# Performance work log

Measured on AMD Instinct MI355X. Metric: run time of the kernel, lower is better.

## Reference

```python
import jax, jax.numpy as jnp
import numpy as np

N_NODES = 10000
N_EDGES = 160000
N_GRAPHS = 20
IN_F, HID, OUT_F, HEADS = 50, 256, 121, 4
NEG_SLOPE = 0.2
GN_EPS = 1e-5
SM_EPS = 1e-16


def _with_self_loops(edge_index, n):
    loop = jnp.arange(n, dtype=edge_index.dtype)
    src = jnp.concatenate([edge_index[0], loop])
    dst = jnp.concatenate([edge_index[1], loop])
    return src, dst


def gat_conv(x, W, att_src, att_dst, bias, src, dst, heads, out_c):
    # PyG GATConv: linear -> per-node attention halves -> edge leaky_relu
    # -> softmax over incoming edges of each dst -> weighted scatter-sum.
    n = x.shape[0]
    h = (x @ W).reshape(n, heads, out_c)                # [N,H,C]
    a_s = (h * att_src).sum(-1)                          # [N,H]
    a_d = (h * att_dst).sum(-1)                          # [N,H]
    e = a_s[src] + a_d[dst]                              # [E,H]
    e = jnp.where(e > 0, e, NEG_SLOPE * e)
    e_max = jax.ops.segment_max(e, dst, num_segments=n)  # self-loops cover all dst
    ex = jnp.exp(e - e_max[dst])
    den = jax.ops.segment_sum(ex, dst, num_segments=n)
    alpha = ex / (den[dst] + SM_EPS)                     # [E,H]
    out = jax.ops.segment_sum(h[src] * alpha[..., None], dst, num_segments=n)
    return out.reshape(n, heads * out_c) + bias


def graph_norm(x, batch, weight, bias, mean_scale, n_graphs):
    cnt = jax.ops.segment_sum(jnp.ones((x.shape[0],), x.dtype), batch,
                              num_segments=n_graphs)[:, None]    # [G,1]
    mean = jax.ops.segment_sum(x, batch, num_segments=n_graphs) / cnt
    ctr = x - mean[batch] * mean_scale
    var = jax.ops.segment_sum(ctr * ctr, batch, num_segments=n_graphs) / cnt
    inv = jax.lax.rsqrt(var + GN_EPS)
    return weight * ctr * inv[batch] + bias


def setup_inputs() -> dict:
    key = jax.random.key(0)
    ks = jax.random.split(key, 24)
    d = {}
    d['x'] = jax.random.normal(ks[0], (N_NODES, IN_F), jnp.float32)
    d['edge_index'] = jax.random.randint(ks[1], (2, N_EDGES), 0, N_NODES, jnp.int64 if jax.config.jax_enable_x64 else jnp.int32)
    d['batch'] = jnp.sort(jax.random.randint(ks[2], (N_NODES,), 0, N_GRAPHS))
    def glorot(k, shape):
        fan = shape[0] + shape[-1]
        return jax.random.normal(k, shape, jnp.float32) * np.sqrt(2.0 / fan)
    dims = [(IN_F, HEADS, HID), (HEADS * HID, HEADS, HID), (HEADS * HID, HEADS, HID), (HEADS * HID, 1, OUT_F)]
    i = 3
    for li, (fin, h, c) in enumerate(dims, 1):
        d[f'W{li}'] = glorot(ks[i], (fin, h * c)); i += 1
        d[f'as{li}'] = glorot(ks[i], (h, c)); i += 1
        d[f'ad{li}'] = glorot(ks[i], (h, c)); i += 1
        d[f'b{li}'] = jnp.zeros((h * c,), jnp.float32)
    for li in (1, 2, 3):
        w = HEADS * HID
        d[f'gw{li}'] = jnp.ones((w,), jnp.float32)
        d[f'gb{li}'] = jnp.zeros((w,), jnp.float32)
        d[f'ga{li}'] = jnp.ones((w,), jnp.float32)
    return d


def reference(x, edge_index, batch,
              W1, as1, ad1, b1, W2, as2, ad2, b2, W3, as3, ad3, b3, W4, as4, ad4, b4,
              gw1, gb1, ga1, gw2, gb2, ga2, gw3, gb3, ga3):
    src, dst = _with_self_loops(edge_index, N_NODES)
    h = gat_conv(x, W1, as1, ad1, b1, src, dst, HEADS, HID)
    h = jax.nn.elu(graph_norm(h, batch, gw1, gb1, ga1, N_GRAPHS))
    h = gat_conv(h, W2, as2, ad2, b2, src, dst, HEADS, HID)
    h = jax.nn.elu(graph_norm(h, batch, gw2, gb2, ga2, N_GRAPHS))
    h = gat_conv(h, W3, as3, ad3, b3, src, dst, HEADS, HID)
    h = jax.nn.elu(graph_norm(h, batch, gw3, gb3, ga3, N_GRAPHS))
    return gat_conv(h, W4, as4, ad4, b4, src, dst, 1, OUT_F)
```

## Files before the change

### kernel.cpp

```cpp
#include <hip/hip_runtime.h>
#include <math.h>

#define NN 10000
#define NE 160000
#define E2 (NE + NN)
#define NG 20
#define MPAD 10240
#define NSPLIT 8

typedef __attribute__((ext_vector_type(8))) short short8;
typedef __attribute__((ext_vector_type(4))) float f32x4;

__device__ inline unsigned short f2bf(float f){
  unsigned u = __float_as_uint(f);
  unsigned r = u + 0x7FFFu + ((u >> 16) & 1u);
  return (unsigned short)(r >> 16);
}
__device__ inline float bf2f(unsigned short h){ return __uint_as_float(((unsigned)h) << 16); }

__device__ inline void gload_lds16(const void* g, void* l){
  __builtin_amdgcn_global_load_lds((const __attribute__((address_space(1))) void*)g,
                                   (__attribute__((address_space(3))) void*)l, 16, 0, 0);
}

__global__ void k_gptr(const int* __restrict__ batch, int* __restrict__ gptr){
  int g = threadIdx.x;
  if (g > NG) return;
  int lo = 0, hi = NN;
  while (lo < hi){ int mid = (lo+hi)>>1; if (batch[mid] < g) lo = mid+1; else hi = mid; }
  gptr[g] = lo;
}

__global__ void k_count(const int* __restrict__ ei, int* __restrict__ cnt){
  int e = blockIdx.x*256 + threadIdx.x;
  if (e >= E2) return;
  int d = (e < NE) ? ei[NE + e] : (e - NE);
  atomicAdd(&cnt[d], 1);
}

__global__ void k_scan(const int* __restrict__ cnt, int* __restrict__ ptr){
  __shared__ int tpre[256];
  __shared__ int tsum[256];
  int tid = threadIdx.x;
  const int per = (NN + 255)/256;
  int base = tid*per;
  int s = 0;
  for (int i=0;i<per;i++){ int idx=base+i; if (idx<NN) s += cnt[idx]; }
  tsum[tid] = s;
  __syncthreads();
  if (tid == 0){
    int run = 0;
    for (int i=0;i<256;i++){ tpre[i]=run; run += tsum[i]; }
    ptr[NN] = run;
  }
  __syncthreads();
  int run = tpre[tid];
  for (int i=0;i<per;i++){ int idx=base+i; if (idx<NN){ ptr[idx]=run; run += cnt[idx]; } }
}

__global__ void k_copy(const int* __restrict__ src, int* __restrict__ dst){
  int i = blockIdx.x*256 + threadIdx.x;
  if (i < NN) dst[i] = src[i];
}

__global__ void k_scatter(const int* __restrict__ ei, int* __restrict__ fill, int* __restrict__ csrc){
  int e = blockIdx.x*256 + threadIdx.x;
  if (e >= E2) return;
  int s, d;
  if (e < NE){ s = ei[e]; d = ei[NE + e]; } else { s = d = e - NE; }
  int pos = atomicAdd(&fill[d], 1);
  csrc[pos] = s;
}

__global__ void k_xconv(const float* __restrict__ x, unsigned short* __restrict__ xbf){
  int i = blockIdx.x*256 + threadIdx.x;
  if (i >= MPAD*64) return;
  int r = i >> 6, c = i & 63;
  float v = (r < NN && c < 50) ? x[r*50 + c] : 0.f;
  xbf[i] = f2bf(v);
}

#define WT0 0
#define WT1 65536
#define WT2 1114112
#define WT3 2162688
#define WTT 2293760
__global__ void k_wconvall(const float* __restrict__ W0, const float* __restrict__ W1,
                           const float* __restrict__ W2, const float* __restrict__ W3,
                           unsigned short* __restrict__ wt){
  int i = blockIdx.x*256 + threadIdx.x;
  if (i >= WTT) return;
  const float* W; int K, N, Kpad, off;
  if (i < WT1){ W=W0; K=50; N=1024; Kpad=64; off=WT0; }
  else if (i < WT2){ W=W1; K=1024; N=1024; Kpad=1024; off=WT1; }
  else if (i < WT3){ W=W2; K=1024; N=1024; Kpad=1024; off=WT2; }
  else { W=W3; K=1024; N=121; Kpad=1024; off=WT3; }
  int j = i - off;
  int nn = j / Kpad, kk = j - nn*Kpad;
  float v = (nn < N && kk < K) ? W[(size_t)kk*N + nn] : 0.f;
  wt[i] = f2bf(v);
}

template<int TBN>
__global__ __launch_bounds__(512, 2) void k_gemm256(
    const unsigned short* __restrict__ A,
    const unsigned short* __restrict__ Bt,
    unsigned short* __restrict__ Cbf,
    int M, int K, int FS, int ncb)
{
  constexpr int MFR = 8;
  constexpr int NFR = TBN/64;
  constexpr int ABYTES = 256*64;
  constexpr int BBYTES = TBN*64;
  constexpr int AINST = 2;
  constexpr int BINST = TBN/128;
  constexpr int LPS = AINST + BINST;
  __shared__ unsigned short sA[3*256*32];
  __shared__ unsigned short sB[3*TBN*32];
  const int tid = threadIdx.x;
  const int wave = tid >> 6;
  const int lane = tid & 63;
  const int nwg = gridDim.x;
  const int q = nwg >> 3, rmod = nwg & 7;
  const int xcd = blockIdx.x & 7, idx = blockIdx.x >> 3;
  const int wg = (xcd < rmod) ? (xcd*(q+1) + idx) : (rmod*(q+1) + (xcd - rmod)*q + idx);
  const int rowt = wg / ncb;
  const int colt = wg - rowt*ncb;
  const int row0 = rowt * 256;
  const int col0 = colt * TBN;
  const int wr = (wave >> 2) * 128;
  const int wc = (wave & 3) * (TBN/4);
  f32x4 acc[MFR][NFR];
  #pragma unroll
  for (int i=0;i<MFR;i++)
    #pragma unroll
    for (int j=0;j<NFR;j++){ acc[i][j][0]=0.f; acc[i][j][1]=0.f; acc[i][j][2]=0.f; acc[i][j][3]=0.f; }

  const unsigned short* aP[AINST];
  int aL[AINST];
  #pragma unroll
  for (int i=0;i<AINST;i++){
    int s = (wave*AINST + i)*64 + lane;
    int row = s >> 2, chn = (s & 3) ^ ((row >> 1) & 3);
    aP[i] = A + (size_t)(row0 + row)*K + chn*8;
    aL[i] = (wave*AINST + i)*1024;
  }
  const unsigned short* bP[BINST];
  int bL[BINST];
  #pragma unroll
  for (int i=0;i<BINST;i++){
    int s = (wave*BINST + i)*64 + lane;
    int row = s >> 2, chn = (s & 3) ^ ((row >> 1) & 3);
    bP[i] = Bt + (size_t)(col0 + row)*K + chn*8;
    bL[i] = (wave*BINST + i)*1024;
  }
  char* ldsA = (char*)sA;
  char* ldsB = (char*)sB;

  auto STAGE = [&](int k0, int buf){
    #pragma unroll
    for (int i=0;i<AINST;i++) gload_lds16(aP[i] + k0, ldsA + buf*ABYTES + aL[i]);
    #pragma unroll
    for (int i=0;i<BINST;i++) gload_lds16(bP[i] + k0, ldsB + buf*BBYTES + bL[i]);
  };

  const int NT = K >> 5;
  const int kch = lane >> 4;
  const int rlo = lane & 15;

  STAGE(0, 0);
  STAGE(32, 1);

  int cur = 0;
  for (int t = 0; t < NT; ++t){
    asm volatile("s_waitcnt lgkmcnt(0)" ::: "memory");
    if (t+1 < NT){
      if constexpr (LPS==4) asm volatile("s_waitcnt vmcnt(4)" ::: "memory");
      else                  asm volatile("s_waitcnt vmcnt(3)" ::: "memory");
    } else {
      asm volatile("s_waitcnt vmcnt(0)" ::: "memory");
    }
    __builtin_amdgcn_sched_barrier(0);
    __builtin_amdgcn_s_barrier();
    __builtin_amdgcn_sched_barrier(0);
    const unsigned short* bA = sA + cur*(256*32);
    const unsigned short* bB = sB + cur*(TBN*32);
    short8 af[MFR], bfr[NFR];
    #pragma unroll
    for (int m=0;m<MFR;m++){
      int r = wr + m*16 + rlo;
      af[m] = *(const short8*)(bA + r*32 + ((kch ^ ((r>>1)&3))<<3));
    }
    #pragma unroll
    for (int n=0;n<NFR;n++){
      int r = wc + n*16 + rlo;
      bfr[n] = *(const short8*)(bB + r*32 + ((kch ^ ((r>>1)&3))<<3));
    }
    if (t+2 < NT){
      int nb = cur + 2; if (nb >= 3) nb -= 3;
      STAGE((t+2) << 5, nb);
    }
    __builtin_amdgcn_s_setprio(1);
    #pragma unroll
    for (int m=0;m<MFR;m++)
      #pragma unroll
      for (int n=0;n<NFR;n++)
        acc[m][n] = __builtin_amdgcn_mfma_f32_16x16x32_bf16(af[m], bfr[n], acc[m][n], 0, 0, 0);
    __builtin_amdgcn_s_setprio(0);
    cur += 1; if (cur == 3) cur = 0;
  }
  const int cr = (lane >> 4) * 4;
  const int cc = lane & 15;
  #pragma unroll
  for (int m=0;m<MFR;m++){
    #pragma unroll
    for (int n=0;n<NFR;n++){
      int col = col0 + wc + n*16 + cc;
      #pragma unroll
      for (int r=0;r<4;r++){
        int row = row0 + wr + m*16 + cr + r;
        if (row < M) Cbf[(size_t)row*FS + col] = f2bf(acc[m][n][r]);
      }
    }
  }
}

__global__ __launch_bounds__(256) void k_attprepw(
    const unsigned short* __restrict__ h,
    const float* __restrict__ atts, const float* __restrict__ attd,
    float* __restrict__ a_s, float* __restrict__ a_d)
{
  const int wid = threadIdx.x >> 6, lane = threadIdx.x & 63;
  const int node = blockIdx.x*4 + wid;
  const unsigned short* hp = h + (size_t)node*1024 + lane*16;
  short8 v0 = *(const short8*)hp;
  short8 v1 = *(const short8*)(hp+8);
  const float* sp = atts + lane*16;
  const float* dp = attd + lane*16;
  float ss = 0.f, sd = 0.f;
  #pragma unroll
  for (int j=0;j<8;j++){ float f = bf2f((unsigned short)v0[j]); ss += f*sp[j];   sd += f*dp[j]; }
  #pragma unroll
  for (int j=0;j<8;j++){ float f = bf2f((unsigned short)v1[j]); ss += f*sp[8+j]; sd += f*dp[8+j]; }
  #pragma unroll
  for (int o=8;o;o>>=1){ ss += __shfl_xor(ss,o); sd += __shfl_xor(sd,o); }
  if ((lane & 15) == 0){
    int hh = lane >> 4;
    a_s[node*4 + hh] = ss;
    a_d[node*4 + hh] = sd;
  }
}

__global__ __launch_bounds__(256) void k_attprep4(
    const unsigned short* __restrict__ h,
    const float* __restrict__ atts, const float* __restrict__ attd,
    float* __restrict__ a_s, float* __restrict__ a_d)
{
  const int wid = threadIdx.x >> 6, lane = threadIdx.x & 63;
  const int node = blockIdx.x*4 + wid;
  const unsigned short* hp = h + (size_t)node*128;
  float ss = 0.f, sd = 0.f;
  {
    float f = bf2f(hp[lane]);
    if (lane < 121){ ss += f*atts[lane]; sd += f*attd[lane]; }
  }
  int c2 = lane + 64;
  if (c2 < 121){
    float f = bf2f(hp[c2]);
    ss += f*atts[c2]; sd += f*attd[c2];
  }
  #pragma unroll
  for (int o=32;o;o>>=1){ ss += __shfl_xor(ss,o); sd += __shfl_xor(sd,o); }
  if (lane == 0){ a_s[node] = ss; a_d[node] = sd; }
}

__global__ __launch_bounds__(256) void k_gatherw(
    const unsigned short* __restrict__ h,
    const float* __restrict__ a_s, const float* __restrict__ a_d,
    const int* __restrict__ ptr, const int* __restrict__ csrc,
    const float* __restrict__ bias, float* __restrict__ out)
{
  __shared__ float sal[4][64*4];
  __shared__ int ssn[4][64];
  const int wid = threadIdx.x >> 6, lane = threadIdx.x & 63;
  const int node = blockIdx.x*4 + wid;
  const int hh = lane >> 4;
  const int beg = ptr[node], deg = ptr[node+1] - beg;
  f32x4 ad4 = *(const f32x4*)(a_d + node*4);
  float acc[16], acc2[16];
  #pragma unroll
  for (int j=0;j<16;j++){ acc[j]=0.f; acc2[j]=0.f; }
  f32x4 denp = {0.f,0.f,0.f,0.f};
  const unsigned short* hb = h + lane*16;

  for (int c0 = 0; c0 < deg; c0 += 64){
    int n = min(64, deg - c0);
    if (lane < n){
      int s = csrc[beg + c0 + lane];
      f32x4 as4 = *(const f32x4*)(a_s + s*4);
      f32x4 e4;
      #pragma unroll
      for (int k2=0;k2<4;k2++){
        float ev = as4[k2] + ad4[k2];
        ev = ev > 0.f ? ev : 0.2f*ev;
        float x = __expf(ev);
        e4[k2] = x;
        denp[k2] += x;
      }
      *(f32x4*)&sal[wid][lane*4] = e4;
      ssn[wid][lane] = s;
    }
    int e = 0;
    for (; e + 1 < n; e += 2){
      int sA_ = ssn[wid][e], sB_ = ssn[wid][e+1];
      float aA = sal[wid][e*4 + hh], aB = sal[wid][(e+1)*4 + hh];
      const unsigned short* pA = hb + (size_t)sA_*1024;
      const unsigned short* pB = hb + (size_t)sB_*1024;
      short8 uA0 = *(const short8*)pA, uA1 = *(const short8*)(pA+8);
      short8 uB0 = *(const short8*)pB, uB1 = *(const short8*)(pB+8);
      #pragma unroll
      for (int j=0;j<8;j++){ acc[j]   += bf2f((unsigned short)uA0[j])*aA;
                             acc[8+j] += bf2f((unsigned short)uA1[j])*aA; }
      #pragma unroll
      for (int j=0;j<8;j++){ acc2[j]   += bf2f((unsigned short)uB0[j])*aB;
                             acc2[8+j] += bf2f((unsigned short)uB1[j])*aB; }
    }
    if (e < n){
      int sA_ = ssn[wid][e];
      float aA = sal[wid][e*4 + hh];
      const unsigned short* pA = hb + (size_t)sA_*1024;
      short8 uA0 = *(const short8*)pA, uA1 = *(const short8*)(pA+8);
      #pragma unroll
      for (int j=0;j<8;j++){ acc[j]   += bf2f((unsigned short)uA0[j])*aA;
                             acc[8+j] += bf2f((unsigned short)uA1[j])*aA; }
    }
  }
  #pragma unroll
  for (int o=32;o;o>>=1){
    #pragma unroll
    for (int k2=0;k2<4;k2++) denp[k2] += __shfl_xor(denp[k2], o);
  }
  float inv = 1.f / (denp[hh] + 1e-16f);
  float* op = out + (size_t)node*1024 + lane*16;
  const float* bp = bias + lane*16;
  #pragma unroll
  for (int j=0;j<16;j++) op[j] = (acc[j]+acc2[j])*inv + bp[j];
}

__global__ __launch_bounds__(256) void k_gatherw1(
    const unsigned short* __restrict__ h,
    const float* __restrict__ a_s, const float* __restrict__ a_d,
    const int* __restrict__ ptr, const int* __restrict__ csrc,
    const float* __restrict__ bias, float* __restrict__ out)
{
  __shared__ float sal[4][64];
  __shared__ int ssn[4][64];
  const int wid = threadIdx.x >> 6, lane = threadIdx.x & 63;
  const int node = blockIdx.x*4 + wid;
  const int beg = ptr[node], deg = ptr[node+1] - beg;
  float ad = a_d[node];
  float den = 0.f;
  float acc[2] = {0.f,0.f}, acc2[2] = {0.f,0.f};
  const int c0i = lane*2;
  const unsigned short* hb = h + c0i;

  for (int b0 = 0; b0 < deg; b0 += 64){
    int n = min(64, deg - b0);
    if (lane < n){
      int s = csrc[beg + b0 + lane];
      float ev = a_s[s] + ad;
      ev = ev > 0.f ? ev : 0.2f*ev;
      float x = __expf(ev);
      sal[wid][lane] = x;
      ssn[wid][lane] = s;
      den += x;
    }
    int e = 0;
    for (; e + 1 < n; e += 2){
      int sA_ = ssn[wid][e], sB_ = ssn[wid][e+1];
      float aA = sal[wid][e], aB = sal[wid][e+1];
      const unsigned short* pA = hb + (size_t)sA_*128;
      const unsigned short* pB = hb + (size_t)sB_*128;
      acc[0]  += bf2f(pA[0])*aA; acc[1]  += bf2f(pA[1])*aA;
      acc2[0] += bf2f(pB[0])*aB; acc2[1] += bf2f(pB[1])*aB;
    }
    if (e < n){
      int sA_ = ssn[wid][e];
      float aA = sal[wid][e];
      const unsigned short* pA = hb + (size_t)sA_*128;
      acc[0] += bf2f(pA[0])*aA; acc[1] += bf2f(pA[1])*aA;
    }
  }
  #pragma unroll
  for (int o=32;o;o>>=1) den += __shfl_xor(den, o);
  float inv = 1.f / (den + 1e-16f);
  if (c0i < 121)   out[(size_t)node*121 + c0i]   = (acc[0]+acc2[0])*inv + bias[c0i];
  if (c0i+1 < 121) out[(size_t)node*121 + c0i+1] = (acc[1]+acc2[1])*inv + bias[c0i+1];
}

__global__ void k_gnstats(const float* __restrict__ x, const int* __restrict__ gptr,
                          float* __restrict__ psum, float* __restrict__ psq){
  int g = blockIdx.x, cc = blockIdx.y, sp = blockIdx.z;
  int c = cc*256 + threadIdx.x;
  int beg = gptr[g], end = gptr[g+1];
  int n = end - beg;
  int per = (n + NSPLIT - 1) / NSPLIT;
  int nb = beg + sp*per, ne = min(end, nb + per);
  float s = 0.f, qv = 0.f;
  for (int i = nb; i < ne; i++){ float v = x[(size_t)i*1024 + c]; s += v; qv += v*v; }
  int idx = (sp*NG + g)*1024 + c;
  psum[idx] = s; psq[idx] = qv;
}

__global__ void k_coef(const float* __restrict__ psum, const float* __restrict__ psq,
                       const int* __restrict__ gptr,
                       const float* __restrict__ w, const float* __restrict__ b, const float* __restrict__ ms,
                       float* __restrict__ cA, float* __restrict__ cB){
  int i = blockIdx.x*256 + threadIdx.x;
  if (i >= NG*1024) return;
  int g = i >> 10, c = i & 1023;
  float cntf = (float)(gptr[g+1] - gptr[g]);
  float sm = 0.f, sq = 0.f;
  #pragma unroll
  for (int sp=0; sp<NSPLIT; sp++){
    sm += psum[(sp*NG + g)*1024 + c];
    sq += psq[(sp*NG + g)*1024 + c];
  }
  float m = sm / cntf;
  float s = ms[c];
  float ex2 = sq / cntf;
  float var = ex2 - 2.f*s*m*m + s*s*m*m;
  float inv = rsqrtf(var + 1e-5f);
  float wa = w[c]*inv;
  cA[i] = wa;
  cB[i] = b[c] - wa*m*s;
}

__global__ void k_applyelu(const float* __restrict__ x, const int* __restrict__ batch,
                           const float* __restrict__ cA, const float* __restrict__ cB,
                           unsigned short* __restrict__ obf){
  size_t i = (size_t)blockIdx.x*256 + threadIdx.x;
  if (i >= (size_t)NN*1024) return;
  int node = (int)(i >> 10);
  int c = (int)(i & 1023);
  int g = batch[node];
  float y = cA[g*1024 + c]*x[i] + cB[g*1024 + c];
  y = y > 0.f ? y : expm1f(y);
  obf[i] = f2bf(y);
}

extern "C" void kernel_launch(void* const* d_in, const int* in_sizes, int n_in,
                              void* d_out, int out_size, void* d_ws, size_t ws_size,
                              hipStream_t stream){
  (void)in_sizes; (void)n_in; (void)out_size; (void)ws_size;
  const float* x     = (const float*)d_in[0];
  const int*   ei    = (const int*)d_in[1];
  const int*   batch = (const int*)d_in[2];
  const float* W[4]  = {(const float*)d_in[3],  (const float*)d_in[7],  (const float*)d_in[11], (const float*)d_in[15]};
  const float* AS[4] = {(const float*)d_in[4],  (const float*)d_in[8],  (const float*)d_in[12], (const float*)d_in[16]};
  const float* AD[4] = {(const float*)d_in[5],  (const float*)d_in[9],  (const float*)d_in[13], (const float*)d_in[17]};
  const float* BI[4] = {(const float*)d_in[6],  (const float*)d_in[10], (const float*)d_in[14], (const float*)d_in[18]};
  const float* GW[3] = {(const float*)d_in[19], (const float*)d_in[22], (const float*)d_in[25]};
  const float* GB[3] = {(const float*)d_in[20], (const float*)d_in[23], (const float*)d_in[26]};
  const float* GA[3] = {(const float*)d_in[21], (const float*)d_in[24], (const float*)d_in[27]};

  float* ws   = (float*)d_ws;
  float* bufB = ws;
  float* a_s  = bufB + (size_t)NN*1024;
  float* a_d  = a_s + (size_t)NN*4;
  float* psum = a_d + (size_t)NN*4;
  float* psq  = psum + (size_t)NSPLIT*NG*1024;
  float* cA   = psq  + (size_t)NSPLIT*NG*1024;
  float* cB   = cA   + (size_t)NG*1024;
  int* ptr  = (int*)(cB + (size_t)NG*1024);
  int* fill = ptr + (NN + 8);
  int* csrc = fill + (NN + 8);
  int* gptr = csrc + E2;
  unsigned short* abf = (unsigned short*)(gptr + 24);
  unsigned short* xbf = abf;
  unsigned short* hbf = abf + (size_t)MPAD*1024;
  unsigned short* wt  = hbf + (size_t)NN*1024;

  hipMemsetAsync(fill, 0, sizeof(int)*(NN+1), stream);
  k_gptr<<<1, 32, 0, stream>>>(batch, gptr);
  k_count<<<(E2+255)/256, 256, 0, stream>>>(ei, fill);
  k_scan<<<1, 256, 0, stream>>>(fill, ptr);
  k_copy<<<(NN+255)/256, 256, 0, stream>>>(ptr, fill);
  k_scatter<<<(E2+255)/256, 256, 0, stream>>>(ei, fill, csrc);
  k_xconv<<<(MPAD*64+255)/256, 256, 0, stream>>>(x, xbf);
  k_wconvall<<<(WTT+255)/256, 256, 0, stream>>>(W[0], W[1], W[2], W[3], wt);

  const int Kp[4]  = {64, 1024, 1024, 1024};
  const int Np[4]  = {1024, 1024, 1024, 128};
  const int Woff[4] = {WT0, WT1, WT2, WT3};
  for (int li = 0; li < 4; ++li){
    int FS = Np[li];
    const unsigned short* Ain = (li == 0) ? xbf : abf;
    const unsigned short* Wt = wt + Woff[li];
    if (li < 3){
      int ncb = 1024/256;
      int nwg = (MPAD/256) * ncb;
      k_gemm256<256><<<nwg, 512, 0, stream>>>(Ain, Wt, hbf, NN, Kp[li], FS, ncb);
      k_attprepw<<<NN/4, 256, 0, stream>>>(hbf, AS[li], AD[li], a_s, a_d);
      k_gatherw<<<NN/4, 256, 0, stream>>>(hbf, a_s, a_d, ptr, csrc, BI[li], bufB);
      k_gnstats<<<dim3(NG, 4, NSPLIT), 256, 0, stream>>>(bufB, gptr, psum, psq);
      k_coef<<<(NG*1024 + 255)/256, 256, 0, stream>>>(psum, psq, gptr, GW[li], GB[li], GA[li], cA, cB);
      k_applyelu<<<(NN*1024 + 255)/256, 256, 0, stream>>>(bufB, batch, cA, cB, abf);
    } else {
      int ncb = 1;
      int nwg = (MPAD/256) * ncb;
      k_gemm256<128><<<nwg, 512, 0, stream>>>(Ain, Wt, hbf, NN, Kp[li], FS, ncb);
      k_attprep4<<<NN/4, 256, 0, stream>>>(hbf, AS[li], AD[li], a_s, a_d);
      k_gatherw1<<<NN/4, 256, 0, stream>>>(hbf, a_s, a_d, ptr, csrc, BI[li], (float*)d_out);
    }
  }
}
```

Before: 502.9 us.

## Fuse attention projections into GEMM epilogue, prefetch gather, vectorize norm kernels

Computes the per-node attention scores a_s/a_d inside the GEMM epilogue from fp32 accumulators, reducing them across waves through shared memory. This removes the separate attprep kernels and their re-read of h. It also software-pipelines the gather loop by loading the next pair of source rows ahead, and vectorizes gnstats and applyelu to 4-wide loads and stores. In exchange, the scores now come from fp32 accumulators rather than bf16-rounded h, which changes numerics slightly. The GEMM epilogue also gains extra syncs and needs more registers.

```diff
diff --git a/kernel.cpp b/kernel.cpp
--- a/kernel.cpp
+++ b/kernel.cpp
@@ -10,6 +10,7 @@
 
 typedef __attribute__((ext_vector_type(8))) short short8;
 typedef __attribute__((ext_vector_type(4))) float f32x4;
+typedef __attribute__((ext_vector_type(4))) unsigned short us4;
 
 __device__ inline unsigned short f2bf(float f){
   unsigned u = __float_as_uint(f);
@@ -101,12 +102,21 @@
   wt[i] = f2bf(v);
 }
 
+__global__ void k_attpad4(const float* __restrict__ AS3, const float* __restrict__ AD3,
+                          float* __restrict__ asp4, float* __restrict__ adp4){
+  int i = threadIdx.x;
+  asp4[i] = (i < 121) ? AS3[i] : 0.f;
+  adp4[i] = (i < 121) ? AD3[i] : 0.f;
+}
+
 template<int TBN>
 __global__ __launch_bounds__(512, 2) void k_gemm256(
     const unsigned short* __restrict__ A,
     const unsigned short* __restrict__ Bt,
     unsigned short* __restrict__ Cbf,
-    int M, int K, int FS, int ncb)
+    const float* __restrict__ asp, const float* __restrict__ adp,
+    float* __restrict__ a_s, float* __restrict__ a_d,
+    int M, int K, int FS, int ncb, int H)
 {
   constexpr int MFR = 8;
   constexpr int NFR = TBN/64;
@@ -223,55 +233,42 @@
       }
     }
   }
-}
-
-__global__ __launch_bounds__(256) void k_attprepw(
-    const unsigned short* __restrict__ h,
-    const float* __restrict__ atts, const float* __restrict__ attd,
-    float* __restrict__ a_s, float* __restrict__ a_d)
-{
-  const int wid = threadIdx.x >> 6, lane = threadIdx.x & 63;
-  const int node = blockIdx.x*4 + wid;
-  const unsigned short* hp = h + (size_t)node*1024 + lane*16;
-  short8 v0 = *(const short8*)hp;
-  short8 v1 = *(const short8*)(hp+8);
-  const float* sp = atts + lane*16;
-  const float* dp = attd + lane*16;
-  float ss = 0.f, sd = 0.f;
-  #pragma unroll
-  for (int j=0;j<8;j++){ float f = bf2f((unsigned short)v0[j]); ss += f*sp[j];   sd += f*dp[j]; }
-  #pragma unroll
-  for (int j=0;j<8;j++){ float f = bf2f((unsigned short)v1[j]); ss += f*sp[8+j]; sd += f*dp[8+j]; }
-  #pragma unroll
-  for (int o=8;o;o>>=1){ ss += __shfl_xor(ss,o); sd += __shfl_xor(sd,o); }
-  if ((lane & 15) == 0){
-    int hh = lane >> 4;
-    a_s[node*4 + hh] = ss;
-    a_d[node*4 + hh] = sd;
-  }
-}
-
-__global__ __launch_bounds__(256) void k_attprep4(
-    const unsigned short* __restrict__ h,
-    const float* __restrict__ atts, const float* __restrict__ attd,
-    float* __restrict__ a_s, float* __restrict__ a_d)
-{
-  const int wid = threadIdx.x >> 6, lane = threadIdx.x & 63;
-  const int node = blockIdx.x*4 + wid;
-  const unsigned short* hp = h + (size_t)node*128;
-  float ss = 0.f, sd = 0.f;
+  float asv[NFR], adv[NFR];
+  #pragma unroll
+  for (int n=0;n<NFR;n++){
+    int col = col0 + wc + n*16 + cc;
+    asv[n] = asp[col]; adv[n] = adp[col];
+  }
+  __syncthreads();
+  float* part = (float*)sA;
+  #pragma unroll
+  for (int m=0;m<MFR;m++){
+    #pragma unroll
+    for (int r=0;r<4;r++){
+      float ss = 0.f, sd = 0.f;
+      #pragma unroll
+      for (int n=0;n<NFR;n++){ float v = acc[m][n][r]; ss += v*asv[n]; sd += v*adv[n]; }
+      #pragma unroll
+      for (int o=8;o;o>>=1){ ss += __shfl_xor(ss,o); sd += __shfl_xor(sd,o); }
+      if (cc == 0){
+        int rowLocal = m*16 + cr + r;
+        int pidx = ((wave>>2)*128 + rowLocal)*8 + (wave&3)*2;
+        part[pidx] = ss; part[pidx+1] = sd;
+      }
+    }
+  }
+  __syncthreads();
   {
-    float f = bf2f(hp[lane]);
-    if (lane < 121){ ss += f*atts[lane]; sd += f*attd[lane]; }
-  }
-  int c2 = lane + 64;
-  if (c2 < 121){
-    float f = bf2f(hp[c2]);
-    ss += f*atts[c2]; sd += f*attd[c2];
-  }
-  #pragma unroll
-  for (int o=32;o;o>>=1){ ss += __shfl_xor(ss,o); sd += __shfl_xor(sd,o); }
-  if (lane == 0){ a_s[node] = ss; a_d[node] = sd; }
+    int row = tid >> 1, v = tid & 1;
+    int base = row*8 + v;
+    float s = part[base] + part[base+2] + part[base+4] + part[base+6];
+    int grow = row0 + row;
+    const int head = colt;
+    if (grow < M){
+      if (v) a_d[grow*H + head] = s;
+      else   a_s[grow*H + head] = s;
+    }
+  }
 }
 
 __global__ __launch_bounds__(256) void k_gatherw(
@@ -311,28 +308,44 @@
       ssn[wid][lane] = s;
     }
     int e = 0;
-    for (; e + 1 < n; e += 2){
-      int sA_ = ssn[wid][e], sB_ = ssn[wid][e+1];
-      float aA = sal[wid][e*4 + hh], aB = sal[wid][(e+1)*4 + hh];
-      const unsigned short* pA = hb + (size_t)sA_*1024;
-      const unsigned short* pB = hb + (size_t)sB_*1024;
-      short8 uA0 = *(const short8*)pA, uA1 = *(const short8*)(pA+8);
-      short8 uB0 = *(const short8*)pB, uB1 = *(const short8*)(pB+8);
-      #pragma unroll
-      for (int j=0;j<8;j++){ acc[j]   += bf2f((unsigned short)uA0[j])*aA;
-                             acc[8+j] += bf2f((unsigned short)uA1[j])*aA; }
-      #pragma unroll
-      for (int j=0;j<8;j++){ acc2[j]   += bf2f((unsigned short)uB0[j])*aB;
-                             acc2[8+j] += bf2f((unsigned short)uB1[j])*aB; }
-    }
-    if (e < n){
-      int sA_ = ssn[wid][e];
-      float aA = sal[wid][e*4 + hh];
-      const unsigned short* pA = hb + (size_t)sA_*1024;
-      short8 uA0 = *(const short8*)pA, uA1 = *(const short8*)(pA+8);
-      #pragma unroll
-      for (int j=0;j<8;j++){ acc[j]   += bf2f((unsigned short)uA0[j])*aA;
-                             acc[8+j] += bf2f((unsigned short)uA1[j])*aA; }
+    if (n >= 2){
+      int s0 = ssn[wid][0], s1 = ssn[wid][1];
+      float aA = sal[wid][hh], aB = sal[wid][4+hh];
+      const unsigned short* p0 = hb + (size_t)s0*1024;
+      const unsigned short* p1 = hb + (size_t)s1*1024;
+      short8 ca0=*(const short8*)p0, ca1=*(const short8*)(p0+8);
+      short8 cb0=*(const short8*)p1, cb1=*(const short8*)(p1+8);
+      for (e = 0; e+3 < n; e += 2){
+        int s2 = ssn[wid][e+2], s3 = ssn[wid][e+3];
+        float nA = sal[wid][(e+2)*4+hh], nB = sal[wid][(e+3)*4+hh];
+        const unsigned short* p2 = hb + (size_t)s2*1024;
+        const unsigned short* p3 = hb + (size_t)s3*1024;
+        short8 na0=*(const short8*)p2, na1=*(const short8*)(p2+8);
+        short8 nb0=*(const short8*)p3, nb1=*(const short8*)(p3+8);
+        #pragma unroll
+        for (int j=0;j<8;j++){ acc[j]   += bf2f((unsigned short)ca0[j])*aA;
+                               acc[8+j] += bf2f((unsigned short)ca1[j])*aA; }
+        #pragma unroll
+        for (int j=0;j<8;j++){ acc2[j]   += bf2f((unsigned short)cb0[j])*aB;
+                               acc2[8+j] += bf2f((unsigned short)cb1[j])*aB; }
+        ca0=na0; ca1=na1; cb0=nb0; cb1=nb1; aA=nA; aB=nB;
+      }
+      #pragma unroll
+      for (int j=0;j<8;j++){ acc[j]   += bf2f((unsigned short)ca0[j])*aA;
+                             acc[8+j] += bf2f((unsigned short)ca1[j])*aA; }
+      #pragma unroll
+      for (int j=0;j<8;j++){ acc2[j]   += bf2f((unsigned short)cb0[j])*aB;
+                             acc2[8+j] += bf2f((unsigned short)cb1[j])*aB; }
+      e += 2;
+    }
+    for (; e < n; ++e){
+      int s = ssn[wid][e];
+      float al = sal[wid][e*4 + hh];
+      const unsigned short* p = hb + (size_t)s*1024;
+      short8 u0 = *(const short8*)p, u1 = *(const short8*)(p+8);
+      #pragma unroll
+      for (int j=0;j<8;j++){ acc[j]   += bf2f((unsigned short)u0[j])*al;
+                             acc[8+j] += bf2f((unsigned short)u1[j])*al; }
     }
   }
   #pragma unroll
@@ -400,16 +413,20 @@
 
 __global__ void k_gnstats(const float* __restrict__ x, const int* __restrict__ gptr,
                           float* __restrict__ psum, float* __restrict__ psq){
-  int g = blockIdx.x, cc = blockIdx.y, sp = blockIdx.z;
-  int c = cc*256 + threadIdx.x;
+  int g = blockIdx.x, sp = blockIdx.z;
+  int c4 = threadIdx.x*4;
   int beg = gptr[g], end = gptr[g+1];
   int n = end - beg;
   int per = (n + NSPLIT - 1) / NSPLIT;
   int nb = beg + sp*per, ne = min(end, nb + per);
-  float s = 0.f, qv = 0.f;
-  for (int i = nb; i < ne; i++){ float v = x[(size_t)i*1024 + c]; s += v; qv += v*v; }
-  int idx = (sp*NG + g)*1024 + c;
-  psum[idx] = s; psq[idx] = qv;
+  f32x4 s = {0.f,0.f,0.f,0.f}, qv = {0.f,0.f,0.f,0.f};
+  for (int i = nb; i < ne; i++){
+    f32x4 v = *(const f32x4*)(x + (size_t)i*1024 + c4);
+    s += v; qv += v*v;
+  }
+  int idx = (sp*NG + g)*1024 + c4;
+  *(f32x4*)(psum + idx) = s;
+  *(f32x4*)(psq + idx) = qv;
 }
 
 __global__ void k_coef(const float* __restrict__ psum, const float* __restrict__ psq,
@@ -439,14 +456,22 @@
 __global__ void k_applyelu(const float* __restrict__ x, const int* __restrict__ batch,
                            const float* __restrict__ cA, const float* __restrict__ cB,
                            unsigned short* __restrict__ obf){
-  size_t i = (size_t)blockIdx.x*256 + threadIdx.x;
-  if (i >= (size_t)NN*1024) return;
-  int node = (int)(i >> 10);
-  int c = (int)(i & 1023);
+  int i = blockIdx.x*256 + threadIdx.x;
+  if (i >= NN*256) return;
+  int node = i >> 8;
+  int c4 = (i & 255)*4;
   int g = batch[node];
-  float y = cA[g*1024 + c]*x[i] + cB[g*1024 + c];
-  y = y > 0.f ? y : expm1f(y);
-  obf[i] = f2bf(y);
+  f32x4 v = *(const f32x4*)(x + (size_t)node*1024 + c4);
+  f32x4 a = *(const f32x4*)(cA + g*1024 + c4);
+  f32x4 b = *(const f32x4*)(cB + g*1024 + c4);
+  us4 o;
+  #pragma unroll
+  for (int j=0;j<4;j++){
+    float y = a[j]*v[j] + b[j];
+    y = y > 0.f ? y : expm1f(y);
+    o[j] = f2bf(y);
+  }
+  *(us4*)(obf + (size_t)node*1024 + c4) = o;
 }
 
 extern "C" void kernel_launch(void* const* d_in, const int* in_sizes, int n_in,
@@ -472,7 +497,9 @@
   float* psq  = psum + (size_t)NSPLIT*NG*1024;
   float* cA   = psq  + (size_t)NSPLIT*NG*1024;
   float* cB   = cA   + (size_t)NG*1024;
-  int* ptr  = (int*)(cB + (size_t)NG*1024);
+  float* asp4 = cB   + (size_t)NG*1024;
+  float* adp4 = asp4 + 128;
+  int* ptr  = (int*)(adp4 + 128);
   int* fill = ptr + (NN + 8);
   int* csrc = fill + (NN + 8);
   int* gptr = csrc + E2;
@@ -489,6 +516,7 @@
   k_scatter<<<(E2+255)/256, 256, 0, stream>>>(ei, fill, csrc);
   k_xconv<<<(MPAD*64+255)/256, 256, 0, stream>>>(x, xbf);
   k_wconvall<<<(WTT+255)/256, 256, 0, stream>>>(W[0], W[1], W[2], W[3], wt);
+  k_attpad4<<<1, 128, 0, stream>>>(AS[3], AD[3], asp4, adp4);
 
   const int Kp[4]  = {64, 1024, 1024, 1024};
   const int Np[4]  = {1024, 1024, 1024, 128};
@@ -498,19 +526,19 @@
     const unsigned short* Ain = (li == 0) ? xbf : abf;
     const unsigned short* Wt = wt + Woff[li];
     if (li < 3){
-      int ncb = 1024/256;
+      int ncb = 4;
       int nwg = (MPAD/256) * ncb;
-      k_gemm256<256><<<nwg, 512, 0, stream>>>(Ain, Wt, hbf, NN, Kp[li], FS, ncb);
-      k_attprepw<<<NN/4, 256, 0, stream>>>(hbf, AS[li], AD[li], a_s, a_d);
+      k_gemm256<256><<<nwg, 512, 0, stream>>>(Ain, Wt, hbf, AS[li], AD[li], a_s, a_d,
+                                              NN, Kp[li], FS, ncb, 4);
       k_gatherw<<<NN/4, 256, 0, stream>>>(hbf, a_s, a_d, ptr, csrc, BI[li], bufB);
-      k_gnstats<<<dim3(NG, 4, NSPLIT), 256, 0, stream>>>(bufB, gptr, psum, psq);
+      k_gnstats<<<dim3(NG, 1, NSPLIT), 256, 0, stream>>>(bufB, gptr, psum, psq);
       k_coef<<<(NG*1024 + 255)/256, 256, 0, stream>>>(psum, psq, gptr, GW[li], GB[li], GA[li], cA, cB);
-      k_applyelu<<<(NN*1024 + 255)/256, 256, 0, stream>>>(bufB, batch, cA, cB, abf);
+      k_applyelu<<<(NN*256 + 255)/256, 256, 0, stream>>>(bufB, batch, cA, cB, abf);
     } else {
       int ncb = 1;
       int nwg = (MPAD/256) * ncb;
-      k_gemm256<128><<<nwg, 512, 0, stream>>>(Ain, Wt, hbf, NN, Kp[li], FS, ncb);
-      k_attprep4<<<NN/4, 256, 0, stream>>>(hbf, AS[li], AD[li], a_s, a_d);
+      k_gemm256<128><<<nwg, 512, 0, stream>>>(Ain, Wt, hbf, asp4, adp4, a_s, a_d,
+                                              NN, Kp[li], FS, ncb, 1);
       k_gatherw1<<<NN/4, 256, 0, stream>>>(hbf, a_s, a_d, ptr, csrc, BI[li], (float*)d_out);
     }
   }
```

Measured after the change: 481.6 us. 1.04x faster.
